# Kernel optimization log

Measured on AMD Instinct MI355X. Metric: run time of the kernel, lower is better.

## Reference

```python
import jax, jax.numpy as jnp
import numpy as np
from jax import lax

K = 3  # dynamic/static conv kernel size
C = 64  # n_feat (hard-coded by Linear(64, ...) in the module)


def leaky(x):
    return jax.nn.leaky_relu(x, 0.1)


def conv2d(x, w, b, pad):
    # x: [B,C,H,W], w: [O,I,kh,kw] (OIHW), b: [O]
    y = lax.conv_general_dilated(x, w, (1, 1), [(pad, pad), (pad, pad)],
                                 dimension_numbers=("NCHW", "OIHW", "NCHW"))
    return y + b.reshape(1, -1, 1, 1)


def rda_conv(x, d, k1, k2, cw, cb):
    # x: [B,C,H,W], d: [B,64]
    b, c, h, w = x.shape
    hid = leaky(d @ k1)                        # [B,64]
    kern = (hid @ k2).reshape(b * c, 1, K, K)  # per-(batch,channel) kernel
    pad = (K - 1) // 2
    # depthwise dynamic conv: groups = b*c
    out = lax.conv_general_dilated(x.reshape(1, b * c, h, w), kern, (1, 1),
                                   [(pad, pad), (pad, pad)],
                                   feature_group_count=b * c,
                                   dimension_numbers=("NCHW", "OIHW", "NCHW"))
    out = leaky(out).reshape(b, c, h, w)
    M = jax.nn.sigmoid(conv2d(x, cw, cb, 0))   # [B,1,H,W] gating map
    return out * M + x


def setup_inputs() -> dict:
    key = jax.random.key(0)
    ks = jax.random.split(key, 14)
    s = 0.05
    inp = {
        "x": jax.random.normal(ks[0], (16, C, 128, 128), jnp.float32),
        "d": jax.random.normal(ks[1], (16, C), jnp.float32),
        # RDA_conv 1: kernel MLP (stored as [in,out]) + 1x1 gating conv
        "da1_k1": jax.random.normal(ks[2], (64, 64), jnp.float32) * s,
        "da1_k2": jax.random.normal(ks[3], (64, 64 * K * K), jnp.float32) * s,
        "da1_cw": jax.random.normal(ks[4], (1, C, 1, 1), jnp.float32) * s,
        "da1_cb": jax.random.normal(ks[5], (1,), jnp.float32) * s,
        # RDA_conv 2
        "da2_k1": jax.random.normal(ks[6], (64, 64), jnp.float32) * s,
        "da2_k2": jax.random.normal(ks[7], (64, 64 * K * K), jnp.float32) * s,
        "da2_cw": jax.random.normal(ks[8], (1, C, 1, 1), jnp.float32) * s,
        "da2_cb": jax.random.normal(ks[9], (1,), jnp.float32) * s,
        # static 3x3 convs
        "conv1_w": jax.random.normal(ks[10], (C, C, K, K), jnp.float32) * s,
        "conv1_b": jax.random.normal(ks[11], (C,), jnp.float32) * s,
        "conv2_w": jax.random.normal(ks[12], (C, C, K, K), jnp.float32) * s,
        "conv2_b": jax.random.normal(ks[13], (C,), jnp.float32) * s,
    }
    return inp


def reference(x, d, da1_k1, da1_k2, da1_cw, da1_cb, da2_k1, da2_k2, da2_cw,
              da2_cb, conv1_w, conv1_b, conv2_w, conv2_b):
    pad = (K - 1) // 2
    out = leaky(rda_conv(x, d, da1_k1, da1_k2, da1_cw, da1_cb))
    out = leaky(conv2d(out, conv1_w, conv1_b, pad))
    out = leaky(rda_conv(out, d, da2_k1, da2_k2, da2_cw, da2_cb))
    out = conv2d(out, conv2_w, conv2_b, pad) + x
    return out
```

## Files before the change

kernel.cpp:

```cpp
#include <hip/hip_runtime.h>
#include <hip/hip_bf16.h>
#include <math.h>

#define B_ 16
#define C_ 64
#define H_ 128
#define W_ 128
#define HW_ (H_*W_)
#define CHW_ (C_*HW_)
#define NTOT_ (B_*CHW_)

typedef __attribute__((ext_vector_type(8))) short short8;
typedef __attribute__((ext_vector_type(4))) float float4v;

__device__ __forceinline__ float leaky(float v) { return v > 0.f ? v : 0.1f * v; }
__device__ __forceinline__ float bs2f(short u) {
    return __uint_as_float(((unsigned)(unsigned short)u) << 16);
}
__device__ __forceinline__ short f2bs(float v) {
    __hip_bfloat16 h = __float2bfloat16(v);
    union { __hip_bfloat16 h; short s; } u; u.h = h; return u.s;
}

__global__ __launch_bounds__(256) void k_setup(
    const float* __restrict__ X, const float* __restrict__ cw,
    const float* __restrict__ cb, __hip_bfloat16* __restrict__ Xn,
    float* __restrict__ G1,
    const float* __restrict__ d,
    const float* __restrict__ k1a, const float* __restrict__ k2a,
    const float* __restrict__ k1b, const float* __restrict__ k2b,
    float* __restrict__ kernA, float* __restrict__ kernB,
    const float* __restrict__ W1, const float* __restrict__ W2,
    __hip_bfloat16* __restrict__ P1, __hip_bfloat16* __restrict__ P2)
{
    __shared__ float sT[64][65];
    __shared__ float pG[4][64];
    __shared__ float hid[64];
    const int bid = blockIdx.x;
    const int tid = threadIdx.x;

    if (bid < 4096) {
        const int b = bid >> 8;
        const int p0 = (bid & 255) * 64;
        #pragma unroll
        for (int i = 0; i < 16; ++i) {
            int idx = i*256 + tid;
            int c = idx >> 6, p = idx & 63;
            sT[c][p] = X[(size_t)b*CHW_ + (size_t)c*HW_ + p0 + p];
        }
        __syncthreads();
        #pragma unroll
        for (int i = 0; i < 16; ++i) {
            int idx = i*256 + tid;
            int p = idx >> 6, c = idx & 63;
            Xn[((size_t)b*HW_ + p0 + p)*64 + c] = __float2bfloat16(sT[c][p]);
        }
        const int cg = tid >> 6, p = tid & 63;
        float part = 0.f;
        #pragma unroll
        for (int c = 0; c < 16; ++c) part = fmaf(sT[cg*16 + c][p], cw[cg*16 + c], part);
        pG[cg][p] = part;
        __syncthreads();
        if (tid < 64) {
            float g = pG[0][tid] + pG[1][tid] + pG[2][tid] + pG[3][tid] + cb[0];
            G1[(size_t)b*HW_ + p0 + tid] = 1.f / (1.f + __expf(-g));
        }
    } else if (bid < 4192) {
        const int r2 = bid - 4096;
        const int which = r2 / 48;
        const int rr    = r2 % 48;
        const int b     = rr / 3;
        const int chunk = rr % 3;
        const float* k1 = which ? k1b : k1a;
        const float* k2 = which ? k2b : k2a;
        float* outp = which ? kernB : kernA;
        if (tid < 64) {
            float s = 0.f;
            #pragma unroll
            for (int i = 0; i < 64; ++i) s = fmaf(d[b*64 + i], k1[i*64 + tid], s);
            hid[tid] = leaky(s);
        }
        __syncthreads();
        if (tid < 192) {
            const int o = chunk * 192 + tid;
            float s = 0.f;
            #pragma unroll
            for (int j = 0; j < 64; ++j) s = fmaf(hid[j], k2[j*576 + o], s);
            outp[b*576 + (o % 9)*64 + (o / 9)] = s;
        }
    } else {
        const int p = bid - 4192;
        const int s = p % 18;
        const int which = p / 18;
        const float* W = which ? W2 : W1;
        __hip_bfloat16* P = which ? P2 : P1;
        const int t = s >> 1, hf = s & 1;
        for (int idx = tid; idx < 2048; idx += 256) {
            const int oc = idx >> 5, kk = idx & 31;
            P[s*2048 + idx] = __float2bfloat16(W[oc*576 + (hf*32 + kk)*9 + t]);
        }
    }
}

template<int MODE>
__global__ __launch_bounds__(512, 2) void k_rda_conv(
    const __hip_bfloat16* __restrict__ Xn, const float* __restrict__ kernN,
    const float* __restrict__ G, const __hip_bfloat16* __restrict__ Wpk,
    const float* __restrict__ bias, const float* __restrict__ Xres,
    const float* __restrict__ Gcw, const float* __restrict__ Gcb,
    __hip_bfloat16* __restrict__ OutN, float* __restrict__ OutF,
    float* __restrict__ G2)
{
    __shared__ __align__(16) short sA[20*20*64];
    const int tid = threadIdx.x;
    const int b = blockIdx.y;
    const int h0 = (blockIdx.x >> 3) * 16;
    const int w0 = (blockIdx.x & 7) * 16;
    const int lane = tid & 63;
    const int wv = tid >> 6;

    const short* Xs = (const short*)Xn;
    for (int idx = tid; idx < 3200; idx += 512) {
        const int cc = idx & 7;
        const int w = (idx >> 3) % 20;
        const int r = idx / 160;
        const int gh = h0 - 2 + r;
        const int gw = w0 - 2 + w;
        uint4 v = make_uint4(0, 0, 0, 0);
        if ((unsigned)gh < (unsigned)H_ && (unsigned)gw < (unsigned)W_)
            v = *(const uint4*)(Xs + (((size_t)b*H_ + gh)*W_ + gw)*64 + cc*8);
        *(uint4*)(sA + ((r*20 + w)*64 + ((cc ^ (w & 7)) * 8))) = v;
    }

    float k9[9];
    #pragma unroll
    for (int t = 0; t < 9; ++t) k9[t] = kernN[((size_t)b*9 + t)*64 + lane];

    int loff[8];
    #pragma unroll
    for (int jc = 0; jc < 8; ++jc)
        loff[jc] = (((lane >> 3) ^ jc) << 3) + (lane & 7);

    auto compute_row = [&](int r, float* outv) {
        const int gh = h0 - 1 + r;
        if ((unsigned)gh < (unsigned)H_) {
            #pragma unroll
            for (int w = 0; w < 18; ++w) outv[w] = 0.f;
            const float* Gp = G + (size_t)b*HW_ + (size_t)gh*W_ + (w0 - 1);
            const short* r0 = sA + (r*20)*64;
            const short* r1 = r0 + 20*64;
            const short* r2 = r1 + 20*64;
            float c1p = 0.f;
            #pragma unroll
            for (int j = 0; j < 20; ++j) {
                const int off = j*64 + loff[j & 7];
                const float c0 = bs2f(r0[off]);
                const float c1 = bs2f(r1[off]);
                const float c2 = bs2f(r2[off]);
                #pragma unroll
                for (int dw = 0; dw < 3; ++dw) {
                    const int w = j - dw;
                    if (w >= 0 && w < 18)
                        outv[w] = fmaf(c0, k9[dw],
                                  fmaf(c1, k9[3+dw],
                                  fmaf(c2, k9[6+dw], outv[w])));
                }
                const int wf = j - 2;
                if (wf >= 0) {
                    const int gw = w0 - 1 + wf;
                    float val = 0.f;
                    if ((unsigned)gw < (unsigned)W_) {
                        const float m = Gp[wf];
                        val = leaky(leaky(outv[wf]) * m + c1p);
                    }
                    outv[wf] = val;
                }
                c1p = c1;
            }
        } else {
            #pragma unroll
            for (int w = 0; w < 18; ++w) outv[w] = 0.f;
        }
    };
    auto write_rowf = [&](int r, const float* ov) {
        short* wp = sA + (r*20)*64;
        #pragma unroll
        for (int w = 0; w < 18; ++w)
            wp[w*64 + loff[w & 7]] = f2bs(ov[w]);
    };

    __syncthreads();

    const int s0 = (wv < 2) ? wv*3 : 6 + (wv - 2)*2;
    const int e  = s0 + ((wv < 2) ? 3 : 2);

    unsigned held0[9], held1[9];
    {
        float outv[18];
        compute_row(e - 2, outv);
        #pragma unroll
        for (int t = 0; t < 9; ++t)
            held0[t] = (unsigned)(unsigned short)f2bs(outv[2*t])
                     | ((unsigned)(unsigned short)f2bs(outv[2*t+1]) << 16);
        compute_row(e - 1, outv);
        #pragma unroll
        for (int t = 0; t < 9; ++t)
            held1[t] = (unsigned)(unsigned short)f2bs(outv[2*t])
                     | ((unsigned)(unsigned short)f2bs(outv[2*t+1]) << 16);
    }
    __syncthreads();

    for (int r = s0; r < e - 2; ++r) {
        float outv[18];
        compute_row(r, outv);
        write_rowf(r, outv);
    }
    {
        short* wp = sA + ((e - 2)*20)*64;
        #pragma unroll
        for (int t = 0; t < 9; ++t) {
            wp[(2*t)*64   + loff[(2*t) & 7]]   = (short)(held0[t] & 0xffff);
            wp[(2*t+1)*64 + loff[(2*t+1) & 7]] = (short)(held0[t] >> 16);
        }
        wp = sA + ((e - 1)*20)*64;
        #pragma unroll
        for (int t = 0; t < 9; ++t) {
            wp[(2*t)*64   + loff[(2*t) & 7]]   = (short)(held1[t] & 0xffff);
            wp[(2*t+1)*64 + loff[(2*t+1) & 7]] = (short)(held1[t] >> 16);
        }
    }
    __syncthreads();

    const int l15 = lane & 15;
    const int lq = lane >> 4;

    float4v acc[2][4];
    #pragma unroll
    for (int i = 0; i < 2; ++i)
        #pragma unroll
        for (int j = 0; j < 4; ++j) acc[i][j] = (float4v)0.f;

    const short* Wp = (const short*)Wpk;

    #pragma unroll
    for (int s = 0; s < 18; ++s) {
        const int t = s >> 1, hf = s & 1;
        const int dh = t / 3, dwx = t % 3;
        short8 afr[2], bfr[4];
        #pragma unroll
        for (int mt = 0; mt < 2; ++mt) {
            const int r = wv*2 + mt + dh;
            const int w = l15 + dwx;
            const int chunk = (hf*4 + lq) ^ (w & 7);
            afr[mt] = *(const short8*)(sA + ((r*20 + w)*64 + chunk*8));
        }
        #pragma unroll
        for (int nt = 0; nt < 4; ++nt)
            bfr[nt] = *(const short8*)(Wp + ((size_t)s*2048 + (nt*16 + l15)*32 + lq*8));
        #pragma unroll
        for (int mt = 0; mt < 2; ++mt)
            #pragma unroll
            for (int nt = 0; nt < 4; ++nt)
                acc[mt][nt] = __builtin_amdgcn_mfma_f32_16x16x32_bf16(
                    afr[mt], bfr[nt], acc[mt][nt], 0, 0, 0);
    }

    float bs[4], cwv[4], cbv = 0.f;
    #pragma unroll
    for (int nt = 0; nt < 4; ++nt) bs[nt] = bias[nt*16 + l15];
    if (MODE == 0) {
        #pragma unroll
        for (int nt = 0; nt < 4; ++nt) cwv[nt] = Gcw[nt*16 + l15];
        cbv = Gcb[0];
    }

    #pragma unroll
    for (int mt = 0; mt < 2; ++mt) {
        const int pr = wv*2 + mt;
        if (MODE == 0) {
            float vv[4][4];
            #pragma unroll
            for (int nt = 0; nt < 4; ++nt)
                #pragma unroll
                for (int rg = 0; rg < 4; ++rg)
                    vv[nt][rg] = leaky(acc[mt][nt][rg] + bs[nt]);
            #pragma unroll
            for (int nt = 0; nt < 4; ++nt) {
                const int n = nt*16 + l15;
                #pragma unroll
                for (int rg = 0; rg < 4; ++rg) {
                    const int pw = lq*4 + rg;
                    OutN[(((size_t)b*H_ + h0 + pr)*W_ + w0 + pw)*64 + n] =
                        __float2bfloat16(vv[nt][rg]);
                }
            }
            #pragma unroll
            for (int rg = 0; rg < 4; ++rg) {
                float p = vv[0][rg]*cwv[0] + vv[1][rg]*cwv[1]
                        + vv[2][rg]*cwv[2] + vv[3][rg]*cwv[3];
                p += __shfl_xor(p, 1);
                p += __shfl_xor(p, 2);
                p += __shfl_xor(p, 4);
                p += __shfl_xor(p, 8);
                if (l15 == 0)
                    G2[(size_t)b*HW_ + (size_t)(h0 + pr)*W_ + w0 + lq*4 + rg] =
                        1.f / (1.f + __expf(-(p + cbv)));
            }
        } else {
            #pragma unroll
            for (int nt = 0; nt < 4; ++nt) {
                const int n = nt*16 + l15;
                const size_t base = ((size_t)(b*64 + n)*H_ + h0 + pr)*W_ + w0 + lq*4;
                const float4 xr = *(const float4*)(Xres + base);
                float4 v;
                v.x = acc[mt][nt][0] + bs[nt] + xr.x;
                v.y = acc[mt][nt][1] + bs[nt] + xr.y;
                v.z = acc[mt][nt][2] + bs[nt] + xr.z;
                v.w = acc[mt][nt][3] + bs[nt] + xr.w;
                *(float4*)(OutF + base) = v;
            }
        }
    }
}

extern "C" void kernel_launch(void* const* d_in, const int* in_sizes, int n_in,
                              void* d_out, int out_size, void* d_ws, size_t ws_size,
                              hipStream_t stream)
{
    const float* x       = (const float*)d_in[0];
    const float* d       = (const float*)d_in[1];
    const float* da1_k1  = (const float*)d_in[2];
    const float* da1_k2  = (const float*)d_in[3];
    const float* da1_cw  = (const float*)d_in[4];
    const float* da1_cb  = (const float*)d_in[5];
    const float* da2_k1  = (const float*)d_in[6];
    const float* da2_k2  = (const float*)d_in[7];
    const float* da2_cw  = (const float*)d_in[8];
    const float* da2_cb  = (const float*)d_in[9];
    const float* conv1_w = (const float*)d_in[10];
    const float* conv1_b = (const float*)d_in[11];
    const float* conv2_w = (const float*)d_in[12];
    const float* conv2_b = (const float*)d_in[13];
    float* out = (float*)d_out;

    __hip_bfloat16* bufA = (__hip_bfloat16*)d_ws;
    __hip_bfloat16* bufB = bufA + NTOT_;
    float* kernA = (float*)(bufB + NTOT_);
    float* kernB = kernA + 16*576;
    __hip_bfloat16* wpk1 = (__hip_bfloat16*)(kernB + 16*576);
    __hip_bfloat16* wpk2 = wpk1 + 18*64*32;
    float* G1 = (float*)(wpk2 + 18*64*32);
    float* G2 = G1 + (size_t)B_*HW_;

    k_setup<<<dim3(4228), dim3(256), 0, stream>>>(
        x, da1_cw, da1_cb, bufA, G1,
        d, da1_k1, da1_k2, da2_k1, da2_k2, kernA, kernB,
        conv1_w, conv2_w, wpk1, wpk2);
    k_rda_conv<0><<<dim3(64, B_), dim3(512), 0, stream>>>(
        bufA, kernA, G1, wpk1, conv1_b, nullptr, da2_cw, da2_cb, bufB, nullptr, G2);
    k_rda_conv<1><<<dim3(64, B_), dim3(512), 0, stream>>>(
        bufB, kernB, G2, wpk2, conv2_b, x, nullptr, nullptr, nullptr, out, nullptr);
}
```

Baseline: 288.2 us.

## Halve block to 4 waves, each computing 4 MFMA row tiles with staged depthwise rounds

Shrinks the fused RDA+conv block from 512 to 256 threads. Each wave now owns four output rows in the MFMA stage instead of two, so every weight B-fragment load is reused across more A tiles. The depthwise phase becomes a round-robin of compute/write rounds with a barrier per round, replacing the held-register scheme. Gating map loads are hoisted ahead of the row loop. The cost is more accumulator registers per thread, fewer waves per block for latency hiding, and extra barriers.

```diff
diff --git a/kernel.cpp b/kernel.cpp
--- a/kernel.cpp
+++ b/kernel.cpp
@@ -103,7 +103,7 @@
 }
 
 template<int MODE>
-__global__ __launch_bounds__(512, 2) void k_rda_conv(
+__global__ __launch_bounds__(256) void k_rda_conv(
     const __hip_bfloat16* __restrict__ Xn, const float* __restrict__ kernN,
     const float* __restrict__ G, const __hip_bfloat16* __restrict__ Wpk,
     const float* __restrict__ bias, const float* __restrict__ Xres,
@@ -120,7 +120,7 @@
     const int wv = tid >> 6;
 
     const short* Xs = (const short*)Xn;
-    for (int idx = tid; idx < 3200; idx += 512) {
+    for (int idx = tid; idx < 3200; idx += 256) {
         const int cc = idx & 7;
         const int w = (idx >> 3) % 20;
         const int r = idx / 160;
@@ -144,9 +144,15 @@
     auto compute_row = [&](int r, float* outv) {
         const int gh = h0 - 1 + r;
         if ((unsigned)gh < (unsigned)H_) {
+            float gv[18];
+            const float* Gp = G + (size_t)b*HW_ + (size_t)gh*W_ + (w0 - 1);
+            #pragma unroll
+            for (int w = 0; w < 18; ++w) {
+                const int gw = w0 - 1 + w;
+                gv[w] = ((unsigned)gw < (unsigned)W_) ? Gp[w] : 0.f;
+            }
             #pragma unroll
             for (int w = 0; w < 18; ++w) outv[w] = 0.f;
-            const float* Gp = G + (size_t)b*HW_ + (size_t)gh*W_ + (w0 - 1);
             const short* r0 = sA + (r*20)*64;
             const short* r1 = r0 + 20*64;
             const short* r2 = r1 + 20*64;
@@ -169,10 +175,8 @@
                 if (wf >= 0) {
                     const int gw = w0 - 1 + wf;
                     float val = 0.f;
-                    if ((unsigned)gw < (unsigned)W_) {
-                        const float m = Gp[wf];
-                        val = leaky(leaky(outv[wf]) * m + c1p);
-                    }
+                    if ((unsigned)gw < (unsigned)W_)
+                        val = leaky(leaky(outv[wf]) * gv[wf] + c1p);
                     outv[wf] = val;
                 }
                 c1p = c1;
@@ -191,52 +195,25 @@
 
     __syncthreads();
 
-    const int s0 = (wv < 2) ? wv*3 : 6 + (wv - 2)*2;
-    const int e  = s0 + ((wv < 2) ? 3 : 2);
-
-    unsigned held0[9], held1[9];
-    {
-        float outv[18];
-        compute_row(e - 2, outv);
-        #pragma unroll
-        for (int t = 0; t < 9; ++t)
-            held0[t] = (unsigned)(unsigned short)f2bs(outv[2*t])
-                     | ((unsigned)(unsigned short)f2bs(outv[2*t+1]) << 16);
-        compute_row(e - 1, outv);
-        #pragma unroll
-        for (int t = 0; t < 9; ++t)
-            held1[t] = (unsigned)(unsigned short)f2bs(outv[2*t])
-                     | ((unsigned)(unsigned short)f2bs(outv[2*t+1]) << 16);
-    }
+    float outv[18];
+    compute_row(wv, outv);
     __syncthreads();
-
-    for (int r = s0; r < e - 2; ++r) {
-        float outv[18];
-        compute_row(r, outv);
-        write_rowf(r, outv);
-    }
-    {
-        short* wp = sA + ((e - 2)*20)*64;
-        #pragma unroll
-        for (int t = 0; t < 9; ++t) {
-            wp[(2*t)*64   + loff[(2*t) & 7]]   = (short)(held0[t] & 0xffff);
-            wp[(2*t+1)*64 + loff[(2*t+1) & 7]] = (short)(held0[t] >> 16);
-        }
-        wp = sA + ((e - 1)*20)*64;
-        #pragma unroll
-        for (int t = 0; t < 9; ++t) {
-            wp[(2*t)*64   + loff[(2*t) & 7]]   = (short)(held1[t] & 0xffff);
-            wp[(2*t+1)*64 + loff[(2*t+1) & 7]] = (short)(held1[t] >> 16);
-        }
-    }
+    #pragma unroll
+    for (int round = 0; round < 4; ++round) {
+        write_rowf(round*4 + wv, outv);
+        const int rn = (round + 1)*4 + wv;
+        if (rn < 18) compute_row(rn, outv);
+        __syncthreads();
+    }
+    if (16 + wv < 18) write_rowf(16 + wv, outv);
     __syncthreads();
 
     const int l15 = lane & 15;
     const int lq = lane >> 4;
 
-    float4v acc[2][4];
-    #pragma unroll
-    for (int i = 0; i < 2; ++i)
+    float4v acc[4][4];
+    #pragma unroll
+    for (int i = 0; i < 4; ++i)
         #pragma unroll
         for (int j = 0; j < 4; ++j) acc[i][j] = (float4v)0.f;
 
@@ -246,10 +223,10 @@
     for (int s = 0; s < 18; ++s) {
         const int t = s >> 1, hf = s & 1;
         const int dh = t / 3, dwx = t % 3;
-        short8 afr[2], bfr[4];
-        #pragma unroll
-        for (int mt = 0; mt < 2; ++mt) {
-            const int r = wv*2 + mt + dh;
+        short8 afr[4], bfr[4];
+        #pragma unroll
+        for (int mt = 0; mt < 4; ++mt) {
+            const int r = wv*4 + mt + dh;
             const int w = l15 + dwx;
             const int chunk = (hf*4 + lq) ^ (w & 7);
             afr[mt] = *(const short8*)(sA + ((r*20 + w)*64 + chunk*8));
@@ -258,7 +235,7 @@
         for (int nt = 0; nt < 4; ++nt)
             bfr[nt] = *(const short8*)(Wp + ((size_t)s*2048 + (nt*16 + l15)*32 + lq*8));
         #pragma unroll
-        for (int mt = 0; mt < 2; ++mt)
+        for (int mt = 0; mt < 4; ++mt)
             #pragma unroll
             for (int nt = 0; nt < 4; ++nt)
                 acc[mt][nt] = __builtin_amdgcn_mfma_f32_16x16x32_bf16(
@@ -275,8 +252,8 @@
     }
 
     #pragma unroll
-    for (int mt = 0; mt < 2; ++mt) {
-        const int pr = wv*2 + mt;
+    for (int mt = 0; mt < 4; ++mt) {
+        const int pr = wv*4 + mt;
         if (MODE == 0) {
             float vv[4][4];
             #pragma unroll
@@ -356,8 +333,8 @@
         x, da1_cw, da1_cb, bufA, G1,
         d, da1_k1, da1_k2, da2_k1, da2_k2, kernA, kernB,
         conv1_w, conv2_w, wpk1, wpk2);
-    k_rda_conv<0><<<dim3(64, B_), dim3(512), 0, stream>>>(
+    k_rda_conv<0><<<dim3(64, B_), dim3(256), 0, stream>>>(
         bufA, kernA, G1, wpk1, conv1_b, nullptr, da2_cw, da2_cb, bufB, nullptr, G2);
-    k_rda_conv<1><<<dim3(64, B_), dim3(512), 0, stream>>>(
+    k_rda_conv<1><<<dim3(64, B_), dim3(256), 0, stream>>>(
         bufB, kernB, G2, wpk2, conv2_b, x, nullptr, nullptr, nullptr, out, nullptr);
 }
```

Result: faster. 249.2 us (-13.5%).
